# Kernel optimization log

Hardware: AMD Instinct MI355X
Metric: run time of the kernel (lower is better)

Reference implementation:

```python
import jax, jax.numpy as jnp
import numpy as np

B, S, H, D = 2, 2048, 16, 64  # batch, seq_len, num_heads, embed_dim(per-head)
DROPOUT_P = 0.1
INV_SCALE = float(D) ** 0.5  # embed_dim ** 0.5, as in the torch module


def setup_inputs() -> dict:
    key = jax.random.key(0)
    ks = jax.random.split(key, 9)
    return {
        "query": jax.random.normal(ks[0], (B, S, H, D), dtype=jnp.float32),
        "key": jax.random.normal(ks[1], (B, S, H, D), dtype=jnp.float32),
        "value": jax.random.normal(ks[2], (B, S, H, D), dtype=jnp.float32),
        "attn_mask": jnp.zeros((B, 1, S, S), dtype=jnp.float32),
        "Wq": jax.random.normal(ks[3], (D, D), dtype=jnp.float32) * (1.0 / np.sqrt(D)),
        "bq": jax.random.normal(ks[4], (D,), dtype=jnp.float32) * 0.02,
        "Wk": jax.random.normal(ks[5], (D, D), dtype=jnp.float32) * (1.0 / np.sqrt(D)),
        "bk": jax.random.normal(ks[6], (D,), dtype=jnp.float32) * 0.02,
        "Wv": jax.random.normal(ks[7], (D, D), dtype=jnp.float32) * (1.0 / np.sqrt(D)),
        "bv": jax.random.normal(ks[8], (D,), dtype=jnp.float32) * 0.02,
    }


def reference(query, key, value, attn_mask, Wq, bq, Wk, bk, Wv, bv):
    # Linear projections on the last (per-head embed) dim, torch Linear: x @ W.T + b
    q = jnp.einsum("bshd,ed->bshe", query, Wq) + bq
    k = jnp.einsum("bshd,ed->bshe", key, Wk) + bk
    v = jnp.einsum("bshd,ed->bshe", value, Wv) + bv
    # permute(0, 2, 1, 3): [B, S, H, D] -> [B, H, S, D]
    q = jnp.transpose(q, (0, 2, 1, 3))
    k = jnp.transpose(k, (0, 2, 1, 3))
    v = jnp.transpose(v, (0, 2, 1, 3))
    # scaled dot-product attention with additive mask
    scores = jnp.einsum("bhqd,bhkd->bhqk", q, k) / INV_SCALE + attn_mask
    attn = jax.nn.softmax(scores, axis=-1)
    # dropout with fixed key (deterministic reference)
    keep = jax.random.bernoulli(jax.random.key(42), 1.0 - DROPOUT_P, attn.shape)
    attn = jnp.where(keep, attn / (1.0 - DROPOUT_P), 0.0)
    # weighted sum of values: [B, H, S, D]
    return jnp.einsum("bhqk,bhkd->bhqd", attn, v)
```

## Files before the change

### kernel.cpp

```cpp
#include <hip/hip_runtime.h>

typedef __attribute__((ext_vector_type(8))) short bf16x8;
typedef __attribute__((ext_vector_type(4))) float f32x4;
typedef __attribute__((ext_vector_type(2))) unsigned u32x2;

#define S_LEN 2048
#define NHEAD 16
#define DHEAD 64

__device__ __forceinline__ short f2bf(float f) {
  unsigned u = __builtin_bit_cast(unsigned, f);
  u += 0x7FFFu + ((u >> 16) & 1u);
  return (short)(u >> 16);
}

__global__ __launch_bounds__(256) void proj_kernel(
    const float* __restrict__ qin, const float* __restrict__ kin,
    const float* __restrict__ vin,
    const float* __restrict__ Wq, const float* __restrict__ bq,
    const float* __restrict__ Wk, const float* __restrict__ bk,
    const float* __restrict__ Wv, const float* __restrict__ bv,
    short* __restrict__ Qp, short* __restrict__ Kp, short* __restrict__ Vp)
{
  const int wid = threadIdx.x >> 6;
  const int lane = threadIdx.x & 63;
  const int lr = lane & 15, lg = lane >> 4;
  const int gw = blockIdx.x * 4 + wid;
  const int tensor = gw >> 10;
  const int rb0 = (gw & 1023) * 64;

  const float* in = tensor == 0 ? qin : (tensor == 1 ? kin : vin);
  const float* W  = tensor == 0 ? Wq  : (tensor == 1 ? Wk  : Wv);
  const float* bb = tensor == 0 ? bq  : (tensor == 1 ? bk  : bv);
  short* op       = tensor == 0 ? Qp  : (tensor == 1 ? Kp  : Vp);

  bf16x8 wf[4][2];
  #pragma unroll
  for (int et = 0; et < 4; ++et)
    #pragma unroll
    for (int h = 0; h < 2; ++h) {
      const float* s = &W[(et*16 + lr)*64 + h*32 + lg*8];
      bf16x8 t;
      #pragma unroll
      for (int e = 0; e < 8; ++e) t[e] = f2bf(s[e]);
      wf[et][h] = t;
    }
  float bias[4];
  #pragma unroll
  for (int et = 0; et < 4; ++et) bias[et] = bb[et*16 + lr];

  for (int blk = 0; blk < 4; ++blk) {
    const int rb = rb0 + blk*16;
    bf16x8 af[2];
    #pragma unroll
    for (int h = 0; h < 2; ++h) {
      const float* s = &in[(size_t)(rb + lr)*64 + h*32 + lg*8];
      bf16x8 t;
      #pragma unroll
      for (int e = 0; e < 8; ++e) t[e] = f2bf(s[e]);
      af[h] = t;
    }
    #pragma unroll
    for (int et = 0; et < 4; ++et) {
      f32x4 acc = {0.f, 0.f, 0.f, 0.f};
      acc = __builtin_amdgcn_mfma_f32_16x16x32_bf16(af[0], wf[et][0], acc, 0, 0, 0);
      acc = __builtin_amdgcn_mfma_f32_16x16x32_bf16(af[1], wf[et][1], acc, 0, 0, 0);
      #pragma unroll
      for (int r = 0; r < 4; ++r) {
        const int row = rb + lg*4 + r;
        const int hh = row & 15;
        const int ss = (row >> 4) & 2047;
        const int bi = row >> 15;
        const size_t orow = ((size_t)(bi*NHEAD + hh))*S_LEN + ss;
        op[orow*64 + et*16 + lr] = f2bf(acc[r] + bias[et]);
      }
    }
  }
}

#define TF_R2(r) \
  xa0 += xa1; xb0 += xb1; \
  xa1 = __builtin_amdgcn_alignbit(xa1, xa1, 32 - (r)) ^ xa0; \
  xb1 = __builtin_amdgcn_alignbit(xb1, xb1, 32 - (r)) ^ xb0;

#define TF_G2(r0, r1, r2, r3) TF_R2(r0) TF_R2(r1) TF_R2(r2) TF_R2(r3)

#define TF_K1 42u
#define TF_K2 (0x1BD11BDAu ^ 42u)
#define TF_THR 3865470464u

#define TF_HASH2(idx, keep0, keep1) { \
  unsigned xa0 = 0u, xa1 = (idx) + TF_K1; \
  unsigned xb0 = 0u, xb1 = (idx) + 16u + TF_K1; \
  TF_G2(13,15,26, 6)  xa0 += TF_K1; xa1 += TF_K2 + 1u;  xb0 += TF_K1; xb1 += TF_K2 + 1u; \
  TF_G2(17,29,16,24)  xa0 += TF_K2; xa1 += 2u;          xb0 += TF_K2; xb1 += 2u; \
  TF_G2(13,15,26, 6)                xa1 += TF_K1 + 3u;                xb1 += TF_K1 + 3u; \
  TF_G2(17,29,16,24)  xa0 += TF_K1; xa1 += TF_K2 + 4u;  xb0 += TF_K1; xb1 += TF_K2 + 4u; \
  TF_G2(13,15,26, 6)  xa0 += TF_K2; xa1 += 5u;          xb0 += TF_K2; xb1 += 5u; \
  keep0 = (xa0 ^ xa1) < TF_THR; \
  keep1 = (xb0 ^ xb1) < TF_THR; \
}

__device__ __forceinline__ unsigned pk_bf16(float lo, float hi) {
  unsigned r;
  asm("v_cvt_pk_bf16_f32 %0, %1, %2" : "=v"(r) : "v"(lo), "v"(hi));
  return r;
}

__global__ __launch_bounds__(256) void attn_kernel(
    const short* __restrict__ Qp, const short* __restrict__ Kp,
    const short* __restrict__ Vp, const float* __restrict__ mask,
    float* __restrict__ out)
{
  __shared__ short Kl[32][72];
  __shared__ short Vt[64][40];
  __shared__ unsigned Pl[4][16][20];

  const int wid = threadIdx.x >> 6;
  const int lane = threadIdx.x & 63;
  const int lr = lane & 15, lg = lane >> 4;
  const int qblk = blockIdx.x >> 5;
  const int bh = blockIdx.x & 31;
  const int b = bh >> 4;
  const int qbase = qblk*64 + wid*16;

  bf16x8 qf[2];
  #pragma unroll
  for (int h = 0; h < 2; ++h)
    qf[h] = *(const bf16x8*)&Qp[((size_t)bh*S_LEN + qbase + lr)*64 + h*32 + lg*8];

  f32x4 acc[4];
  #pragma unroll
  for (int dt = 0; dt < 4; ++dt) acc[dt] = (f32x4){0.f,0.f,0.f,0.f};
  float m_run = -1e30f;
  float l_run = 0.f;

  const float* mrow_p = mask + (size_t)b*S_LEN*S_LEN + (size_t)(qbase + lr)*S_LEN;
  const unsigned rowbase = ((unsigned)(bh*S_LEN + qbase + lr)) << 11;

  const int tr = threadIdx.x >> 3;
  const int tc = (threadIdx.x & 7) * 8;
  const int vswz = tr ^ (8*((tc >> 3) & 3));
  const short* kvbase = &Kp[((size_t)bh*S_LEN + tr)*64 + tc];
  const short* vvbase = &Vp[((size_t)bh*S_LEN + tr)*64 + tc];

  bf16x8 kv = *(const bf16x8*)(kvbase);
  bf16x8 vv = *(const bf16x8*)(vvbase);

  for (int kt = 0; kt < 64; ++kt) {
    const int kb = kt * 32;
    *(bf16x8*)&Kl[tr][tc] = kv;
    #pragma unroll
    for (int j = 0; j < 8; ++j) Vt[tc + j][vswz] = vv[j];
    __syncthreads();

    {
      const int kbn = (kt < 63) ? (kb + 32) : kb;
      kv = *(const bf16x8*)(kvbase + (size_t)kbn*64);
      vv = *(const bf16x8*)(vvbase + (size_t)kbn*64);
    }

    f32x4 mk0 = *(const f32x4*)(mrow_p + kb + lg*4);
    f32x4 mk1 = *(const f32x4*)(mrow_p + kb + 16 + lg*4);

    float km0[4], km1[4];
    #pragma unroll
    for (int r = 0; r < 4; ++r) {
      bool k0, k1;
      TF_HASH2(rowbase + (unsigned)(kb + lg*4 + r), k0, k1);
      km0[r] = k0 ? (1.0f/0.9f) : 0.0f;
      km1[r] = k1 ? (1.0f/0.9f) : 0.0f;
    }

    f32x4 sc0, sc1;
    {
      bf16x8 ka = *(const bf16x8*)&Kl[lr][lg*8];
      bf16x8 kb_ = *(const bf16x8*)&Kl[lr][32 + lg*8];
      f32x4 t = {0.f,0.f,0.f,0.f};
      t = __builtin_amdgcn_mfma_f32_16x16x32_bf16(ka, qf[0], t, 0, 0, 0);
      t = __builtin_amdgcn_mfma_f32_16x16x32_bf16(kb_, qf[1], t, 0, 0, 0);
      sc0 = t;
      bf16x8 kc = *(const bf16x8*)&Kl[16 + lr][lg*8];
      bf16x8 kd = *(const bf16x8*)&Kl[16 + lr][32 + lg*8];
      f32x4 u = {0.f,0.f,0.f,0.f};
      u = __builtin_amdgcn_mfma_f32_16x16x32_bf16(kc, qf[0], u, 0, 0, 0);
      u = __builtin_amdgcn_mfma_f32_16x16x32_bf16(kd, qf[1], u, 0, 0, 0);
      sc1 = u;
    }

    float x0[4], x1[4];
    #pragma unroll
    for (int r = 0; r < 4; ++r) {
      x0[r] = sc0[r] * 0.125f + mk0[r];
      x1[r] = sc1[r] * 0.125f + mk1[r];
    }
    float tm = fmaxf(fmaxf(fmaxf(x0[0], x0[1]), fmaxf(x0[2], x0[3])),
                     fmaxf(fmaxf(x1[0], x1[1]), fmaxf(x1[2], x1[3])));
    tm = fmaxf(tm, __shfl_xor(tm, 16));
    tm = fmaxf(tm, __shfl_xor(tm, 32));
    const float mnew = fmaxf(m_run, tm);
    const float corr = __expf(m_run - mnew);
    m_run = mnew;
    float p0[4], p1[4];
    #pragma unroll
    for (int r = 0; r < 4; ++r) {
      p0[r] = __expf(x0[r] - mnew);
      p1[r] = __expf(x1[r] - mnew);
    }
    float rs = ((p0[0]+p0[1]) + (p0[2]+p0[3])) + ((p1[0]+p1[1]) + (p1[2]+p1[3]));
    rs += __shfl_xor(rs, 16);
    rs += __shfl_xor(rs, 32);
    l_run = l_run * corr + rs;

    const unsigned w0 = pk_bf16(p0[0]*km0[0], p0[1]*km0[1]);
    const unsigned w1 = pk_bf16(p0[2]*km0[2], p0[3]*km0[3]);
    const unsigned w2 = pk_bf16(p1[0]*km1[0], p1[1]*km1[1]);
    const unsigned w3 = pk_bf16(p1[2]*km1[2], p1[3]*km1[3]);
    *(u32x2*)&Pl[wid][lr][lg*2]     = (u32x2){w0, w1};
    *(u32x2*)&Pl[wid][lr][8 + lg*2] = (u32x2){w2, w3};
    asm volatile("" ::: "memory");

    #pragma unroll
    for (int r = 0; r < 4; ++r) {
      const float c = __shfl(corr, lg*4 + r);
      #pragma unroll
      for (int dt = 0; dt < 4; ++dt) acc[dt][r] *= c;
    }

    bf16x8 pf = *(const bf16x8*)&Pl[wid][lr][lg*4];
    #pragma unroll
    for (int dt = 0; dt < 4; ++dt) {
      const int vc = (lg ^ ((dt*2 + (lr >> 3)) & 3)) * 8;
      bf16x8 vf = *(const bf16x8*)&Vt[dt*16 + lr][vc];
      acc[dt] = __builtin_amdgcn_mfma_f32_16x16x32_bf16(pf, vf, acc[dt], 0, 0, 0);
    }
    __syncthreads();
  }

  #pragma unroll
  for (int r = 0; r < 4; ++r) {
    const int qrow = qbase + lg*4 + r;
    const float linv = 1.0f / __shfl(l_run, lg*4 + r);
    #pragma unroll
    for (int dt = 0; dt < 4; ++dt)
      out[((size_t)bh*S_LEN + qrow)*64 + dt*16 + lr] = acc[dt][r] * linv;
  }
}

extern "C" void kernel_launch(void* const* d_in, const int* in_sizes, int n_in,
                              void* d_out, int out_size, void* d_ws, size_t ws_size,
                              hipStream_t stream) {
  const float* qin  = (const float*)d_in[0];
  const float* kin  = (const float*)d_in[1];
  const float* vin  = (const float*)d_in[2];
  const float* mask = (const float*)d_in[3];
  const float* Wq = (const float*)d_in[4];
  const float* bq = (const float*)d_in[5];
  const float* Wk = (const float*)d_in[6];
  const float* bk = (const float*)d_in[7];
  const float* Wv = (const float*)d_in[8];
  const float* bv = (const float*)d_in[9];
  float* out = (float*)d_out;

  short* Qp = (short*)d_ws;
  short* Kp = Qp + 4194304;
  short* Vp = Kp + 4194304;

  hipLaunchKernelGGL(proj_kernel, dim3(768), dim3(256), 0, stream,
                     qin, kin, vin, Wq, bq, Wk, bk, Wv, bv, Qp, Kp, Vp);
  hipLaunchKernelGGL(attn_kernel, dim3(1024), dim3(256), 0, stream,
                     Qp, Kp, Vp, mask, out);
}
```

Measured before the change: 481.2 us.

## Double-buffer K/V tiles in LDS to drop one barrier per iteration

Splits the K and V shared-memory tiles into two buffers. Each iteration now writes the next tile into the alternate buffer while computing on the current one, so only one __syncthreads per iteration is needed instead of two. Global prefetch moves two tiles ahead, and the launch bounds add a minimum-occupancy hint of 4 blocks per CU with unroll 2. The cost is twice the LDS for K and V plus tighter register limits, which could cause spills.

```diff
diff --git a/kernel.cpp b/kernel.cpp
--- a/kernel.cpp
+++ b/kernel.cpp
@@ -107,13 +107,13 @@
   return r;
 }
 
-__global__ __launch_bounds__(256) void attn_kernel(
+__global__ __launch_bounds__(256, 4) void attn_kernel(
     const short* __restrict__ Qp, const short* __restrict__ Kp,
     const short* __restrict__ Vp, const float* __restrict__ mask,
     float* __restrict__ out)
 {
-  __shared__ short Kl[32][72];
-  __shared__ short Vt[64][40];
+  __shared__ short Kl[2][32][72];
+  __shared__ short Vt[2][64][40];
   __shared__ unsigned Pl[4][16][20];
 
   const int wid = threadIdx.x >> 6;
@@ -146,19 +146,25 @@
 
   bf16x8 kv = *(const bf16x8*)(kvbase);
   bf16x8 vv = *(const bf16x8*)(vvbase);
-
+  *(bf16x8*)&Kl[0][tr][tc] = kv;
+  #pragma unroll
+  for (int j = 0; j < 8; ++j) Vt[0][tc + j][vswz] = vv[j];
+  kv = *(const bf16x8*)(kvbase + 32*64);
+  vv = *(const bf16x8*)(vvbase + 32*64);
+  __syncthreads();
+
+  #pragma unroll 2
   for (int kt = 0; kt < 64; ++kt) {
+    const int cur = kt & 1, nxt = cur ^ 1;
     const int kb = kt * 32;
-    *(bf16x8*)&Kl[tr][tc] = kv;
-    #pragma unroll
-    for (int j = 0; j < 8; ++j) Vt[tc + j][vswz] = vv[j];
-    __syncthreads();
-
-    {
-      const int kbn = (kt < 63) ? (kb + 32) : kb;
-      kv = *(const bf16x8*)(kvbase + (size_t)kbn*64);
-      vv = *(const bf16x8*)(vvbase + (size_t)kbn*64);
-    }
+
+    *(bf16x8*)&Kl[nxt][tr][tc] = kv;
+    #pragma unroll
+    for (int j = 0; j < 8; ++j) Vt[nxt][tc + j][vswz] = vv[j];
+
+    const int kbn = (kt < 62) ? (kb + 64) : 2016;
+    kv = *(const bf16x8*)(kvbase + (size_t)kbn*64);
+    vv = *(const bf16x8*)(vvbase + (size_t)kbn*64);
 
     f32x4 mk0 = *(const f32x4*)(mrow_p + kb + lg*4);
     f32x4 mk1 = *(const f32x4*)(mrow_p + kb + 16 + lg*4);
@@ -174,14 +180,14 @@
 
     f32x4 sc0, sc1;
     {
-      bf16x8 ka = *(const bf16x8*)&Kl[lr][lg*8];
-      bf16x8 kb_ = *(const bf16x8*)&Kl[lr][32 + lg*8];
+      bf16x8 ka = *(const bf16x8*)&Kl[cur][lr][lg*8];
+      bf16x8 kb_ = *(const bf16x8*)&Kl[cur][lr][32 + lg*8];
       f32x4 t = {0.f,0.f,0.f,0.f};
       t = __builtin_amdgcn_mfma_f32_16x16x32_bf16(ka, qf[0], t, 0, 0, 0);
       t = __builtin_amdgcn_mfma_f32_16x16x32_bf16(kb_, qf[1], t, 0, 0, 0);
       sc0 = t;
-      bf16x8 kc = *(const bf16x8*)&Kl[16 + lr][lg*8];
-      bf16x8 kd = *(const bf16x8*)&Kl[16 + lr][32 + lg*8];
+      bf16x8 kc = *(const bf16x8*)&Kl[cur][16 + lr][lg*8];
+      bf16x8 kd = *(const bf16x8*)&Kl[cur][16 + lr][32 + lg*8];
       f32x4 u = {0.f,0.f,0.f,0.f};
       u = __builtin_amdgcn_mfma_f32_16x16x32_bf16(kc, qf[0], u, 0, 0, 0);
       u = __builtin_amdgcn_mfma_f32_16x16x32_bf16(kd, qf[1], u, 0, 0, 0);
@@ -231,7 +237,7 @@
     #pragma unroll
     for (int dt = 0; dt < 4; ++dt) {
       const int vc = (lg ^ ((dt*2 + (lr >> 3)) & 3)) * 8;
-      bf16x8 vf = *(const bf16x8*)&Vt[dt*16 + lr][vc];
+      bf16x8 vf = *(const bf16x8*)&Vt[cur][dt*16 + lr][vc];
       acc[dt] = __builtin_amdgcn_mfma_f32_16x16x32_bf16(pf, vf, acc[dt], 0, 0, 0);
     }
     __syncthreads();
```

New measurement: 427.8 us. 11.1% less time.
